# Kernel tuning notes

Hardware: AMD Instinct MI355X
Metric: run time of the kernel (lower is better)

## Reference

```python
import jax, jax.numpy as jnp
import numpy as np

K = 7
PAD = K // 2
SIG_L = (4.0, 6.0, 8.0)
SIG_S = (1.0, 2.0, 3.0)
DORD = (0, 1, 2)
ANG = (1, 2, 3, 4)
N_INV, N_EQ, N_CP = 8, 16, 16
LN_EPS = 1e-5


def _polar_grid(k):
    c = jnp.arange(k, dtype=jnp.float32) - (k - 1) / 2.0
    gy, gx = jnp.meshgrid(c, c, indexing='ij')
    r = jnp.sqrt(gx * gx + gy * gy + 1e-8)
    th = jnp.arctan2(gy, gx)
    return r, th


def _gaussian_basis(r, sigmas, orders, n):
    # Gaussian-derivative radial basis (Eqs. 13-14): cycle over (order, sigma) combos.
    combos = [(s, d) for d in orders for s in sigmas]
    mats = []
    for i in range(n):
        s, d = combos[i % len(combos)]
        u = r / s
        g = jnp.exp(-0.5 * u * u)
        p = jnp.ones_like(u) if d == 0 else (u if d == 1 else u * u - 1.0)
        psi = p * g
        mats.append(psi / jnp.sqrt(jnp.sum(psi * psi) + 1e-8))
    return jnp.stack(mats)  # [n, K, K]


def _harmonic_basis(r, th, w1, b1, w2, b2, n):
    # Circular harmonics (Eqs. 15-16): learnable radial MLP x cos/sin(n*theta).
    kk = r.size
    rad = jnp.tanh(r.reshape(kk, 1) @ w1 + b1) @ w2 + b2  # [K*K, M]
    tf = th.reshape(kk)
    ang = jnp.stack([f(o * tf) for o in ANG for f in (jnp.cos, jnp.sin)])  # [2L, K*K]
    basis = (rad.T[:, None, :] * ang[None, :, :]).reshape(-1, K, K)  # [M*2L, K, K]
    return basis[:n]


def _coeff(z, w1, b1, w2, b2, n, cout):
    h = jax.nn.relu(z @ w1 + b1)
    return (h @ w2 + b2).reshape(z.shape[0], n, cout)  # [B, N, C_out]


def _pconv(feature, kernel):
    # Per-sample kernel shared across input channels: conv2d with weight
    # expand over C_in == conv of the channel-sum with the per-(b,o) kernel.
    B, Cin, H, W = feature.shape
    Cout = kernel.shape[1]
    fs = feature.sum(axis=1)[None]  # [1, B, H, W]
    rhs = kernel.reshape(B * Cout, 1, K, K)
    out = jax.lax.conv_general_dilated(fs, rhs, (1, 1), [(PAD, PAD), (PAD, PAD)], feature_group_count=B)
    return out.reshape(B, Cout, H, W)


def _ln_c(x, g, b):
    # LayerNorm over channel dim (permute(0,2,3,1) -> LN -> permute back)
    mu = jnp.mean(x, axis=1, keepdims=True)
    var = jnp.var(x, axis=1, keepdims=True)
    return (x - mu) * jax.lax.rsqrt(var + LN_EPS) * g[None, :, None, None] + b[None, :, None, None]


def setup_inputs() -> dict:
    key = jax.random.key(0)
    ks = jax.random.split(key, 16)
    B, C, H, W = 16, 256, 48, 48
    hid = 64
    d = {}
    d['feature'] = jax.random.normal(ks[0], (B, C, H, W), jnp.float32)
    for i, (name, n) in enumerate([('inv', N_INV), ('eq', N_EQ), ('cp', N_CP)]):
        d[f'cg_{name}_w1'] = jax.random.normal(ks[1 + 4 * i], (C, hid), jnp.float32) * 0.05
        d[f'cg_{name}_b1'] = jnp.zeros((hid,), jnp.float32)
        d[f'cg_{name}_w2'] = jax.random.normal(ks[2 + 4 * i], (hid, n * C), jnp.float32) * 0.05
        d[f'cg_{name}_b2'] = jnp.zeros((n * C,), jnp.float32)
    d['rad_w1'] = jax.random.normal(ks[13], (1, 32), jnp.float32)
    d['rad_b1'] = jnp.zeros((32,), jnp.float32)
    d['rad_w2'] = jax.random.normal(ks[14], (32, 2), jnp.float32) * 0.3
    d['rad_b2'] = jnp.zeros((2,), jnp.float32)
    for name in ('inv', 'eq', 'cp'):
        d[f'ln_{name}_g'] = jnp.ones((C,), jnp.float32)
        d[f'ln_{name}_b'] = jnp.zeros((C,), jnp.float32)
    return d


def reference(feature, cg_inv_w1, cg_inv_b1, cg_inv_w2, cg_inv_b2,
              cg_eq_w1, cg_eq_b1, cg_eq_w2, cg_eq_b2,
              cg_cp_w1, cg_cp_b1, cg_cp_w2, cg_cp_b2,
              rad_w1, rad_b1, rad_w2, rad_b2,
              ln_inv_g, ln_inv_b, ln_eq_g, ln_eq_b, ln_cp_g, ln_cp_b):
    C_out = ln_inv_g.shape[0]
    r, th = _polar_grid(K)
    b_inv = _gaussian_basis(r, SIG_L, DORD, N_INV)
    b_eq = _gaussian_basis(r, SIG_S, DORD, N_EQ)
    b_cp = _harmonic_basis(r, th, rad_w1, rad_b1, rad_w2, rad_b2, N_CP)
    z = feature.mean(axis=(2, 3))  # [B, C] global average pool
    # Eq. 12: kernel[b,c] = sum_n coeff[b,n,c] * basis[n]
    k_inv = jnp.einsum('bnc,nhw->bchw', _coeff(z, cg_inv_w1, cg_inv_b1, cg_inv_w2, cg_inv_b2, N_INV, C_out), b_inv)
    k_eq = jnp.einsum('bnc,nhw->bchw', _coeff(z, cg_eq_w1, cg_eq_b1, cg_eq_w2, cg_eq_b2, N_EQ, C_out), b_eq)
    k_cp = jnp.einsum('bnc,nhw->bchw', _coeff(z, cg_cp_w1, cg_cp_b1, cg_cp_w2, cg_cp_b2, N_CP, C_out), b_cp)
    f_inv = _ln_c(_pconv(feature, k_inv), ln_inv_g, ln_inv_b)
    f_eq = _ln_c(_pconv(feature, k_eq), ln_eq_g, ln_eq_b)
    f_cp = _ln_c(_pconv(feature, k_cp), ln_cp_g, ln_cp_b)
    return (f_inv, f_eq, f_cp)
```

## Files before the change

### kernel.cpp

```cpp
#include <hip/hip_runtime.h>

#define B_ 16
#define C_ 256
#define H_ 48
#define W_ 48
#define HW_ 2304

typedef float f4 __attribute__((ext_vector_type(4)));

#define WS_ZPART 0
#define WS_FSPART 36864
#define WS_FSPAD 184320
#define WS_BASIS 232704
#define WS_COEFFT 234784
#define WS_MQ 431392
#define WS_CMEAN 443680
#define WS_H 444448
#define WS_G 447520

__device__ __forceinline__ float wave_sum(float v) {
#pragma unroll
  for (int off = 32; off; off >>= 1) v += __shfl_xor(v, off, 64);
  return v;
}

__global__ __launch_bounds__(256) void zfs1_kernel(const float* __restrict__ feat,
                                                   float* __restrict__ zpart,
                                                   float* __restrict__ fspart) {
  int b = blockIdx.x, cc = blockIdx.y, pc = blockIdx.z;
  int tid = threadIdx.x;
  int p = pc * 256 + tid;
  const float* f = feat + ((size_t)b * C_ + cc * 64) * HW_ + p;
  __shared__ float zsum[256];
  int w = tid >> 6, lane = tid & 63;
  float facc = 0.f;
#pragma unroll 8
  for (int j = 0; j < 64; ++j) {
    float v = f[(size_t)j * HW_];
    facc += v;
    float s = wave_sum(v);
    if (lane == 0) zsum[w * 64 + j] = s;
  }
  fspart[cc * (B_ * HW_) + b * HW_ + p] = facc;
  __syncthreads();
  if (tid < 64) {
    float zv = zsum[tid] + zsum[64 + tid] + zsum[128 + tid] + zsum[192 + tid];
    zpart[((size_t)b * 256 + cc * 64 + tid) * 9 + pc] = zv;
  }
}

__global__ __launch_bounds__(256) void prep_kernel(
    const float* __restrict__ fspart, const float* __restrict__ zpart,
    const float* __restrict__ rw1, const float* __restrict__ rb1,
    const float* __restrict__ rw2, const float* __restrict__ rb2,
    const float* __restrict__ w1i, const float* __restrict__ b1i,
    const float* __restrict__ w1e, const float* __restrict__ b1e,
    const float* __restrict__ w1c, const float* __restrict__ b1c,
    float* __restrict__ fspad, float* __restrict__ basis,
    float* __restrict__ hout) {
  int bx = blockIdx.x, tid = threadIdx.x;
  if (bx < 16) {
    int b = bx;
    for (int i = tid; i < 54 * 56; i += 256) {
      int yy = i / 56;
      int xx = i - yy * 56;
      int y = yy - 3, x = xx - 3;
      float v = 0.f;
      if (y >= 0 && y < H_ && x >= 0 && x < W_) {
        int idx = b * HW_ + y * W_ + x;
        v = fspart[idx] + fspart[B_ * HW_ + idx] + fspart[2 * B_ * HW_ + idx] +
            fspart[3 * B_ * HW_ + idx];
      }
      fspad[b * 3024 + i] = v;
    }
    return;
  }
  if (bx < 56) {
    if (tid >= 64) return;
    int t = tid;
    float r = 0.f, th = 0.f;
    if (t < 49) {
      int iy = t / 7, ix = t - iy * 7;
      float gy = (float)iy - 3.f, gx = (float)ix - 3.f;
      r = sqrtf(gx * gx + gy * gy + 1e-8f);
      th = atan2f(gy, gx);
    }
    if (bx < 40) {
      int f = bx - 16;
      const float SIGL[3] = {4.f, 6.f, 8.f};
      const float SIGS[3] = {1.f, 2.f, 3.f};
      int i = (f < 8) ? f : f - 8;
      int c = i % 9, d = c / 3;
      float s = (f < 8) ? SIGL[c % 3] : SIGS[c % 3];
      float p = 0.f;
      if (t < 49) {
        float u = r / s;
        float g = expf(-0.5f * u * u);
        p = ((d == 0) ? 1.f : ((d == 1) ? u : (u * u - 1.f))) * g;
      }
      float ss = wave_sum(p * p);
      if (t < 49) basis[f * 52 + t] = p / sqrtf(ss + 1e-8f);
    } else if (t < 49) {
      int i = bx - 40;
      float r0 = rb2[0], r1 = rb2[1];
      for (int j = 0; j < 32; ++j) {
        float h = tanhf(r * rw1[j] + rb1[j]);
        r0 = fmaf(h, rw2[2 * j], r0);
        r1 = fmaf(h, rw2[2 * j + 1], r1);
      }
      int m = i >> 3, a = i & 7, o = (a >> 1) + 1;
      float ang = (a & 1) ? sinf((float)o * th) : cosf((float)o * th);
      basis[(24 + i) * 52 + t] = (m ? r1 : r0) * ang;
    }
    return;
  }
  int idx = bx - 56;
  int branch = idx >> 4, b = idx & 15;
  const float* w1 = branch == 0 ? w1i : (branch == 1 ? w1e : w1c);
  const float* b1 = branch == 0 ? b1i : (branch == 1 ? b1e : b1c);
  __shared__ float zs[256], hp[256];
  {
    const float* zp = zpart + ((size_t)b * 256 + tid) * 9;
    float za = 0.f;
#pragma unroll
    for (int i = 0; i < 9; ++i) za += zp[i];
    zs[tid] = za * (1.f / (float)HW_);
  }
  __syncthreads();
  int j = tid & 63, part = tid >> 6;
  float acc = 0.f;
  const float* wp = w1 + part * 64 * 64 + j;
#pragma unroll
  for (int q = 0; q < 64; ++q) acc = fmaf(zs[part * 64 + q], wp[q * 64], acc);
  hp[tid] = acc;
  __syncthreads();
  if (tid < 64)
    hout[idx * 64 + tid] = fmaxf(
        b1[tid] + hp[tid] + hp[64 + tid] + hp[128 + tid] + hp[192 + tid], 0.f);
}

__global__ __launch_bounds__(256) void gca_kernel(
    const float* __restrict__ fspad, const float* __restrict__ basis,
    const float* __restrict__ hbuf, const float* __restrict__ w2i,
    const float* __restrict__ b2i, const float* __restrict__ w2e,
    const float* __restrict__ b2e, const float* __restrict__ w2c,
    const float* __restrict__ b2c, float* __restrict__ G,
    float* __restrict__ coeffT) {
  int tid = threadIdx.x;
  if (blockIdx.x < 640) {
    int j = blockIdx.x;
    int b = j / 40, ng = j - b * 40;
    int c = tid;
    int branch = (ng < 8) ? 0 : ((ng < 24) ? 1 : 2);
    int nl = ng - ((branch == 0) ? 0 : ((branch == 1) ? 8 : 24));
    int Nc = (branch == 0) ? 8 : 16;
    const float* w2 = branch == 0 ? w2i : (branch == 1 ? w2e : w2c);
    const float* b2 = branch == 0 ? b2i : (branch == 1 ? b2e : b2c);
    __shared__ float hs[64];
    if (c < 64) hs[c] = hbuf[(branch * 16 + b) * 64 + c];
    __syncthreads();
    float acc = b2[nl * 256 + c];
    const float* wp = w2 + (size_t)nl * 256 + c;
    size_t stride = (size_t)Nc * 256;
#pragma unroll
    for (int jj = 0; jj < 64; ++jj) acc = fmaf(hs[jj], wp[jj * stride], acc);
    float* ctp = coeffT + ((size_t)(b * 3 + branch) * 256 + c) * 16;
    ctp[nl] = acc;
    if (branch == 0) ctp[nl + 8] = 0.f;
    return;
  }
  int i = blockIdx.x - 640;
  int ng = i / 144;
  int r = i - ng * 144;
  int b = r / 9, pc = r - b * 9;
  int p = pc * 256 + tid;
  int py = p / 48, px = p - py * 48;
  const float* wb = fspad + b * 3024 + py * 56 + px;
  float wreg[49];
#pragma unroll
  for (int dy = 0; dy < 7; ++dy)
#pragma unroll
    for (int dx = 0; dx < 7; ++dx) wreg[dy * 7 + dx] = wb[dy * 56 + dx];
  float* go = G + ((size_t)b * 40 + ng * 10) * HW_ + p;
#pragma unroll 2
  for (int ni = 0; ni < 10; ++ni) {
    const float* bs = basis + (ng * 10 + ni) * 52;
    float acc = 0.f;
#pragma unroll
    for (int k = 0; k < 49; ++k) acc = fmaf(bs[k], wreg[k], acc);
    go[(size_t)ni * HW_] = acc;
  }
}

__global__ __launch_bounds__(256) void mstat_kernel(
    const float* __restrict__ coeffT, float* __restrict__ Mq,
    float* __restrict__ cmean) {
  int b = blockIdx.x, branch = blockIdx.y, tid = threadIdx.x;
  __shared__ float Ls[4096];
  const float* base = coeffT + (size_t)(b * 3 + branch) * 4096;
#pragma unroll
  for (int k = 0; k < 16; ++k) Ls[k * 256 + tid] = base[k * 256 + tid];
  __syncthreads();
  int nn = tid >> 4, mm = tid & 15;
  float dot = 0.f;
#pragma unroll 8
  for (int cc = 0; cc < 256; ++cc)
    dot = fmaf(Ls[((cc & 15) * 16 + (cc >> 4)) * 16 + nn],
               Ls[((cc & 15) * 16 + (cc >> 4)) * 16 + mm], dot);
  Mq[(b * 3 + branch) * 256 + tid] = dot * (1.f / 256.f);
  if (tid < 16) {
    float s = 0.f;
    for (int cc = 0; cc < 256; ++cc) s += Ls[cc * 16 + tid];
    cmean[(b * 3 + branch) * 16 + tid] = s * (1.f / 256.f);
  }
}

__global__ __launch_bounds__(256) void pout_kernel(
    const float* __restrict__ G, const float* __restrict__ coeffT,
    const float* __restrict__ Mq, const float* __restrict__ cmean,
    const float* __restrict__ g0, const float* __restrict__ be0,
    const float* __restrict__ g1, const float* __restrict__ be1,
    const float* __restrict__ g2, const float* __restrict__ be2,
    float* __restrict__ out) {
  int branch = blockIdx.y;
  int bx = blockIdx.x;
  int b = bx / 36, pc = bx - b * 36;
  int p0 = pc * 64;
  int tid = threadIdx.x;
  int n0 = (branch == 0) ? 0 : ((branch == 1) ? 8 : 24);
  __shared__ __align__(16) float Ms[256];
  __shared__ float cms[16];
  __shared__ __align__(16) float smu[64];
  __shared__ __align__(16) float srs[64];
  Ms[tid] = Mq[(b * 3 + branch) * 256 + tid];
  if (tid < 16) cms[tid] = cmean[(b * 3 + branch) * 16 + tid];
  __syncthreads();
  if (tid < 64) {
    int p = p0 + tid;
    float gr[16];
#pragma unroll
    for (int n = 0; n < 16; ++n)
      gr[n] = G[((size_t)b * 40 + n0 + n) * HW_ + p];
    float mu = 0.f, q = 0.f;
#pragma unroll
    for (int n = 0; n < 16; ++n) {
      mu = fmaf(cms[n], gr[n], mu);
      float t = 0.f;
#pragma unroll
      for (int m = 0; m < 16; ++m) t = fmaf(Ms[n * 16 + m], gr[m], t);
      q = fmaf(gr[n], t, q);
    }
    smu[tid] = mu;
    srs[tid] = rsqrtf(q - mu * mu + 1e-5f);
  }
  __syncthreads();
  int pg = tid & 7, cg = tid >> 3;
  int c0 = cg * 8;
  const float* gp = (branch == 0) ? g0 : ((branch == 1) ? g1 : g2);
  const float* bp = (branch == 0) ? be0 : ((branch == 1) ? be1 : be2);
  float gch[8], bch[8];
#pragma unroll
  for (int i = 0; i < 8; ++i) {
    gch[i] = gp[c0 + i];
    bch[i] = bp[c0 + i];
  }
  const f4* ct4 =
      reinterpret_cast<const f4*>(coeffT + ((size_t)(b * 3 + branch) * 256 + c0) * 16);
#pragma unroll
  for (int half = 0; half < 2; ++half) {
    int p = p0 + half * 32 + pg * 4;
    f4 Gr[16];
#pragma unroll
    for (int n = 0; n < 16; ++n)
      Gr[n] =
          *reinterpret_cast<const f4*>(G + ((size_t)b * 40 + n0 + n) * HW_ + p);
    f4 mu4 = *reinterpret_cast<const f4*>(smu + half * 32 + pg * 4);
    f4 rs4 = *reinterpret_cast<const f4*>(srs + half * 32 + pg * 4);
    float* op = out + ((size_t)((branch * 16 + b) * 256 + c0)) * HW_ + p;
#pragma unroll
    for (int ci = 0; ci < 8; ++ci) {
      f4 a = ct4[ci * 4 + 0], bb = ct4[ci * 4 + 1];
      f4 cc = ct4[ci * 4 + 2], dd = ct4[ci * 4 + 3];
      f4 v = a.x * Gr[0];
      v += a.y * Gr[1];
      v += a.z * Gr[2];
      v += a.w * Gr[3];
      v += bb.x * Gr[4];
      v += bb.y * Gr[5];
      v += bb.z * Gr[6];
      v += bb.w * Gr[7];
      v += cc.x * Gr[8];
      v += cc.y * Gr[9];
      v += cc.z * Gr[10];
      v += cc.w * Gr[11];
      v += dd.x * Gr[12];
      v += dd.y * Gr[13];
      v += dd.z * Gr[14];
      v += dd.w * Gr[15];
      f4 o = (v - mu4) * rs4;
      o = o * gch[ci] + bch[ci];
      __builtin_nontemporal_store(o,
                                  reinterpret_cast<f4*>(op + (size_t)ci * HW_));
    }
  }
}

extern "C" void kernel_launch(void* const* d_in, const int* in_sizes, int n_in,
                              void* d_out, int out_size, void* d_ws,
                              size_t ws_size, hipStream_t stream) {
  const float* feat = (const float*)d_in[0];
  float* ws = (float*)d_ws;
  float* zpart = ws + WS_ZPART;
  float* fspart = ws + WS_FSPART;
  float* fspad = ws + WS_FSPAD;
  float* basis = ws + WS_BASIS;
  float* coeffT = ws + WS_COEFFT;
  float* Mq = ws + WS_MQ;
  float* cmean = ws + WS_CMEAN;
  float* hbuf = ws + WS_H;
  float* G = ws + WS_G;

  zfs1_kernel<<<dim3(16, 4, 9), 256, 0, stream>>>(feat, zpart, fspart);
  prep_kernel<<<104, 256, 0, stream>>>(
      fspart, zpart, (const float*)d_in[13], (const float*)d_in[14],
      (const float*)d_in[15], (const float*)d_in[16], (const float*)d_in[1],
      (const float*)d_in[2], (const float*)d_in[5], (const float*)d_in[6],
      (const float*)d_in[9], (const float*)d_in[10], fspad, basis, hbuf);
  gca_kernel<<<1216, 256, 0, stream>>>(
      fspad, basis, hbuf, (const float*)d_in[3], (const float*)d_in[4],
      (const float*)d_in[7], (const float*)d_in[8], (const float*)d_in[11],
      (const float*)d_in[12], G, coeffT);
  mstat_kernel<<<dim3(16, 3), 256, 0, stream>>>(coeffT, Mq, cmean);
  pout_kernel<<<dim3(16 * 36, 3), 256, 0, stream>>>(
      G, coeffT, Mq, cmean, (const float*)d_in[17], (const float*)d_in[18],
      (const float*)d_in[19], (const float*)d_in[20], (const float*)d_in[21],
      (const float*)d_in[22], (float*)d_out);
}
```

Baseline: 258.5 us.

## Split LayerNorm stats into separate kernel and restructure output kernel tiling

Measured after the change: 461.8 us. 78.7% more time.

```diff
diff --git a/kernel.cpp b/kernel.cpp
--- a/kernel.cpp
+++ b/kernel.cpp
@@ -11,6 +11,8 @@
 #define WS_ZPART 0
 #define WS_FSPART 36864
 #define WS_FSPAD 184320
+#define WS_MU 0
+#define WS_RS 110592
 #define WS_BASIS 232704
 #define WS_COEFFT 234784
 #define WS_MQ 431392
@@ -215,47 +217,49 @@
   }
 }
 
+__global__ __launch_bounds__(256) void lnstat_kernel(
+    const float* __restrict__ G, const float* __restrict__ Mq,
+    const float* __restrict__ cmean, float* __restrict__ mu_,
+    float* __restrict__ rs_) {
+  int b = blockIdx.x, branch = blockIdx.y, pc = blockIdx.z;
+  int tid = threadIdx.x;
+  __shared__ float Ms[256];
+  __shared__ float cms[16];
+  Ms[tid] = Mq[(b * 3 + branch) * 256 + tid];
+  if (tid < 16) cms[tid] = cmean[(b * 3 + branch) * 16 + tid];
+  __syncthreads();
+  int p = pc * 256 + tid;
+  int n0 = (branch == 0) ? 0 : ((branch == 1) ? 8 : 24);
+  float gr[16];
+#pragma unroll
+  for (int n = 0; n < 16; ++n) gr[n] = G[((size_t)b * 40 + n0 + n) * HW_ + p];
+  float mu = 0.f, q = 0.f;
+#pragma unroll
+  for (int n = 0; n < 16; ++n) {
+    mu = fmaf(cms[n], gr[n], mu);
+    float t = 0.f;
+#pragma unroll
+    for (int m = 0; m < 16; ++m) t = fmaf(Ms[n * 16 + m], gr[m], t);
+    q = fmaf(gr[n], t, q);
+  }
+  mu_[(size_t)(b * 3 + branch) * HW_ + p] = mu;
+  rs_[(size_t)(b * 3 + branch) * HW_ + p] = rsqrtf(q - mu * mu + 1e-5f);
+}
+
 __global__ __launch_bounds__(256) void pout_kernel(
     const float* __restrict__ G, const float* __restrict__ coeffT,
-    const float* __restrict__ Mq, const float* __restrict__ cmean,
+    const float* __restrict__ mu_, const float* __restrict__ rs_,
     const float* __restrict__ g0, const float* __restrict__ be0,
     const float* __restrict__ g1, const float* __restrict__ be1,
     const float* __restrict__ g2, const float* __restrict__ be2,
     float* __restrict__ out) {
+  int bx = blockIdx.x;
   int branch = blockIdx.y;
-  int bx = blockIdx.x;
-  int b = bx / 36, pc = bx - b * 36;
-  int p0 = pc * 64;
+  int b = bx >> 3, cch = bx & 7;
   int tid = threadIdx.x;
+  int wave = tid >> 6, lane = tid & 63;
+  int c0 = cch * 32 + wave * 8;
   int n0 = (branch == 0) ? 0 : ((branch == 1) ? 8 : 24);
-  __shared__ __align__(16) float Ms[256];
-  __shared__ float cms[16];
-  __shared__ __align__(16) float smu[64];
-  __shared__ __align__(16) float srs[64];
-  Ms[tid] = Mq[(b * 3 + branch) * 256 + tid];
-  if (tid < 16) cms[tid] = cmean[(b * 3 + branch) * 16 + tid];
-  __syncthreads();
-  if (tid < 64) {
-    int p = p0 + tid;
-    float gr[16];
-#pragma unroll
-    for (int n = 0; n < 16; ++n)
-      gr[n] = G[((size_t)b * 40 + n0 + n) * HW_ + p];
-    float mu = 0.f, q = 0.f;
-#pragma unroll
-    for (int n = 0; n < 16; ++n) {
-      mu = fmaf(cms[n], gr[n], mu);
-      float t = 0.f;
-#pragma unroll
-      for (int m = 0; m < 16; ++m) t = fmaf(Ms[n * 16 + m], gr[m], t);
-      q = fmaf(gr[n], t, q);
-    }
-    smu[tid] = mu;
-    srs[tid] = rsqrtf(q - mu * mu + 1e-5f);
-  }
-  __syncthreads();
-  int pg = tid & 7, cg = tid >> 3;
-  int c0 = cg * 8;
   const float* gp = (branch == 0) ? g0 : ((branch == 1) ? g1 : g2);
   const float* bp = (branch == 0) ? be0 : ((branch == 1) ? be1 : be2);
   float gch[8], bch[8];
@@ -264,23 +268,24 @@
     gch[i] = gp[c0 + i];
     bch[i] = bp[c0 + i];
   }
-  const f4* ct4 =
-      reinterpret_cast<const f4*>(coeffT + ((size_t)(b * 3 + branch) * 256 + c0) * 16);
-#pragma unroll
-  for (int half = 0; half < 2; ++half) {
-    int p = p0 + half * 32 + pg * 4;
+  const float* Gb = G + ((size_t)b * 40 + n0) * HW_;
+  const float* ctb = coeffT + ((size_t)(b * 3 + branch) * 256 + c0) * 16;
+  const float* mub = mu_ + (size_t)(b * 3 + branch) * HW_;
+  const float* rsb = rs_ + (size_t)(b * 3 + branch) * HW_;
+  float* ob = out + ((size_t)((branch * 16 + b) * 256 + c0)) * HW_;
+#pragma unroll 1
+  for (int pc = 0; pc < 9; ++pc) {
+    int p = pc * 256 + lane * 4;
     f4 Gr[16];
 #pragma unroll
     for (int n = 0; n < 16; ++n)
-      Gr[n] =
-          *reinterpret_cast<const f4*>(G + ((size_t)b * 40 + n0 + n) * HW_ + p);
-    f4 mu4 = *reinterpret_cast<const f4*>(smu + half * 32 + pg * 4);
-    f4 rs4 = *reinterpret_cast<const f4*>(srs + half * 32 + pg * 4);
-    float* op = out + ((size_t)((branch * 16 + b) * 256 + c0)) * HW_ + p;
-#pragma unroll
-    for (int ci = 0; ci < 8; ++ci) {
-      f4 a = ct4[ci * 4 + 0], bb = ct4[ci * 4 + 1];
-      f4 cc = ct4[ci * 4 + 2], dd = ct4[ci * 4 + 3];
+      Gr[n] = *reinterpret_cast<const f4*>(Gb + (size_t)n * HW_ + p);
+    f4 mu4 = *reinterpret_cast<const f4*>(mub + p);
+    f4 rs4 = *reinterpret_cast<const f4*>(rsb + p);
+#pragma unroll
+    for (int j = 0; j < 8; ++j) {
+      const f4* ct4 = reinterpret_cast<const f4*>(ctb + j * 16);
+      f4 a = ct4[0], bb = ct4[1], cc = ct4[2], dd = ct4[3];
       f4 v = a.x * Gr[0];
       v += a.y * Gr[1];
       v += a.z * Gr[2];
@@ -297,10 +302,9 @@
       v += dd.y * Gr[13];
       v += dd.z * Gr[14];
       v += dd.w * Gr[15];
-      f4 o = (v - mu4) * rs4;
-      o = o * gch[ci] + bch[ci];
+      f4 o = (v - mu4) * rs4 * gch[j] + bch[j];
       __builtin_nontemporal_store(o,
-                                  reinterpret_cast<f4*>(op + (size_t)ci * HW_));
+                                  reinterpret_cast<f4*>(ob + (size_t)j * HW_ + p));
     }
   }
 }
@@ -313,6 +317,8 @@
   float* zpart = ws + WS_ZPART;
   float* fspart = ws + WS_FSPART;
   float* fspad = ws + WS_FSPAD;
+  float* mu_ = ws + WS_MU;
+  float* rs_ = ws + WS_RS;
   float* basis = ws + WS_BASIS;
   float* coeffT = ws + WS_COEFFT;
   float* Mq = ws + WS_MQ;
@@ -331,8 +337,9 @@
       (const float*)d_in[7], (const float*)d_in[8], (const float*)d_in[11],
       (const float*)d_in[12], G, coeffT);
   mstat_kernel<<<dim3(16, 3), 256, 0, stream>>>(coeffT, Mq, cmean);
-  pout_kernel<<<dim3(16 * 36, 3), 256, 0, stream>>>(
-      G, coeffT, Mq, cmean, (const float*)d_in[17], (const float*)d_in[18],
+  lnstat_kernel<<<dim3(16, 3, 9), 256, 0, stream>>>(G, Mq, cmean, mu_, rs_);
+  pout_kernel<<<dim3(16 * 8, 3), 256, 0, stream>>>(
+      G, coeffT, mu_, rs_, (const float*)d_in[17], (const float*)d_in[18],
       (const float*)d_in[19], (const float*)d_in[20], (const float*)d_in[21],
       (const float*)d_in[22], (float*)d_out);
 }
```
